# Optimization experiments

Measured on AMD Instinct MI355X. Metric: run time of the kernel, lower is better.

The kernel has to match this reference:

```python
import jax, jax.numpy as jnp
import numpy as np

HEADS = 12
KEY_DIM = 16
B, C, H, W = 16, 384, 64, 64


def _hard_swish(x):
    return x * jnp.clip(x + 3.0, 0.0, 6.0) / 6.0


def _affine(x, g, b):
    # Inference-mode BatchNorm folded into per-channel scale/shift (NCHW).
    return x * g[:, None, None] + b[:, None, None]


def _pw(x, w):
    # 1x1 conv as a channel contraction: x [B,Cin,H,W], w [Cout,Cin].
    return jnp.einsum('bchw,oc->bohw', x, w)


def setup_inputs() -> dict:
    key = jax.random.key(0)
    ks = jax.random.split(key, 20)
    d = {}
    d['x'] = jax.random.normal(ks[0], (B, C, H, W), dtype=jnp.float32)
    d['rnd_offset'] = jax.random.uniform(ks[1], (B, 2, 1, 1), dtype=jnp.float32) * 6.0 - 3.0
    S = HEADS * KEY_DIM  # 192
    d['proj_w'] = jax.random.normal(ks[2], (3 * S, C + 2), dtype=jnp.float32) * 0.05
    d['proj_g'] = jax.random.uniform(ks[3], (3 * S,), dtype=jnp.float32) + 0.5
    d['proj_b'] = jax.random.normal(ks[4], (3 * S,), dtype=jnp.float32) * 0.1
    d['vp2_w'] = jax.random.normal(ks[5], (C, S), dtype=jnp.float32) * 0.05
    d['vp2_g'] = jax.random.uniform(ks[6], (C,), dtype=jnp.float32) + 0.5
    d['vp2_b'] = jax.random.normal(ks[7], (C,), dtype=jnp.float32) * 0.1
    d['dw_w'] = jax.random.normal(ks[8], (C, 1, 5, 5), dtype=jnp.float32) * 0.1
    d['dw_g'] = jax.random.uniform(ks[9], (C,), dtype=jnp.float32) + 0.5
    d['dw_b'] = jax.random.normal(ks[10], (C,), dtype=jnp.float32) * 0.1
    d['pw1_w'] = jax.random.normal(ks[11], (4 * C, C), dtype=jnp.float32) * 0.05
    d['pw1_g'] = jax.random.uniform(ks[12], (4 * C,), dtype=jnp.float32) + 0.5
    d['pw1_b'] = jax.random.normal(ks[13], (4 * C,), dtype=jnp.float32) * 0.1
    d['pw2_w'] = jax.random.normal(ks[14], (C, 4 * C), dtype=jnp.float32) * 0.05
    d['out_g'] = jax.random.uniform(ks[15], (C,), dtype=jnp.float32) + 0.5
    d['out_b'] = jax.random.normal(ks[16], (C,), dtype=jnp.float32) * 0.1
    d['rz_attn'] = jnp.float32(0.1)
    d['rz_ffn'] = jnp.float32(0.1)
    d['embed_strength'] = jnp.float32(-10.0)
    return d


def reference(x, rnd_offset, proj_w, proj_g, proj_b, vp2_w, vp2_g, vp2_b,
              dw_w, dw_g, dw_b, pw1_w, pw1_g, pw1_b, pw2_w, out_g, out_b,
              rz_attn, rz_ffn, embed_strength):
    b, c, h, w = x.shape
    # --- learned-strength positional embedding with random per-image offset ---
    xp = jnp.arange(w, dtype=x.dtype) / 1000.0
    yp = jnp.arange(h, dtype=x.dtype) / 1000.0
    xx, yy = jnp.meshgrid(xp, yp, indexing='xy')      # each (H, W)
    pos = jnp.stack([xx, yy], axis=0)[None]           # (1, 2, H, W)
    pos = jnp.exp(embed_strength) * (pos + rnd_offset)  # (B, 2, H, W)
    x_emb = jnp.concatenate([x, pos], axis=1)         # (B, C+2, H, W)

    # --- qkv projection (1x1 conv + BN + ReLU), computed in fp32 ---
    proj = jax.nn.relu(_affine(_pw(x_emb, proj_w), proj_g, proj_b))
    proj = proj.astype(jnp.float32)

    S = HEADS * KEY_DIM
    N = h * w

    def get_slice(i):
        # (B, S, H, W) slice -> (B*heads, N, key_dim)
        s = proj[:, i * S:(i + 1) * S]
        return s.reshape(b * HEADS, KEY_DIM, N).transpose(0, 2, 1)

    q, k, v = get_slice(0), get_slice(1), get_slice(2)

    # --- non-causal linear attention: Q (K^T V) / (Q sum(K)) ---
    ktv = jnp.einsum('bnd,bne->bde', k, v)            # (B*heads, d, d)
    numer = jnp.einsum('bnd,bde->bne', q, ktv)        # (B*heads, N, d)
    denom = jnp.einsum('bnd,bd->bn', q, k.sum(axis=1))[..., None]  # (B*heads, N, 1)
    out = numer / jnp.maximum(denom, 1e-4)
    out = out.transpose(0, 2, 1).reshape(b, S, h, w)  # (B, heads*key_dim, H, W)

    # --- value projection back to channels ---
    out = jax.nn.relu(_affine(_pw(out, vp2_w), vp2_g, vp2_b))
    y = x + rz_attn * out

    # --- FFN: depthwise 5x5 -> expand 1x1 -> project 1x1 (+ BNs) ---
    z = jax.lax.conv_general_dilated(
        y, dw_w, window_strides=(1, 1), padding='SAME',
        dimension_numbers=('NCHW', 'OIHW', 'NCHW'), feature_group_count=c)
    z = _hard_swish(_affine(z, dw_g, dw_b))
    z = _hard_swish(_affine(_pw(z, pw1_w), pw1_g, pw1_b))
    z = _affine(_pw(z, pw2_w), out_g, out_b)
    return y + rz_ffn * z
```

## Files before the change

kernel.cpp:

```cpp
#include <hip/hip_runtime.h>
#include <cstdint>

typedef unsigned short u16;
typedef __attribute__((ext_vector_type(8))) __bf16 bf16x8;
typedef __attribute__((ext_vector_type(4))) float f32x4;

__device__ __forceinline__ u16 f2bf(float f) {
    union { float f; uint32_t u; } v; v.f = f;
    uint32_t u = v.u;
    uint32_t r = (u + 0x7fffu + ((u >> 16) & 1u)) >> 16;
    return (u16)r;
}
__device__ __forceinline__ float bf2f(u16 h) {
    union { uint32_t u; float f; } v; v.u = ((uint32_t)h) << 16;
    return v.f;
}

__device__ __forceinline__ void ld_lds16(const u16* g, u16* l) {
    __builtin_amdgcn_global_load_lds(
        (const __attribute__((address_space(1))) uint32_t*)g,
        (__attribute__((address_space(3))) uint32_t*)l, 16, 0, 0);
}

__global__ __launch_bounds__(256) void prep(
    const float* __restrict__ proj_w, const float* __restrict__ proj_g,
    const float* __restrict__ proj_b, const float* __restrict__ vp2_w,
    const float* __restrict__ pw1_w, const float* __restrict__ pw2_w,
    const float* __restrict__ dw_w,
    u16* __restrict__ w1p, u16* __restrict__ w2, u16* __restrict__ w3,
    u16* __restrict__ w4, float* __restrict__ gp, float2* __restrict__ dwp)
{
    int i = blockIdx.x * 256 + threadIdx.x;
    if (i < 245760) {
        int o = i / 384, k = i - o * 384;
        w1p[i] = (o < 576) ? f2bf(proj_w[o * 386 + k]) : (u16)0;
        return;
    }
    i -= 245760;
    if (i < 73728) { w2[i] = f2bf(vp2_w[i]); return; }
    i -= 73728;
    if (i < 589824) { w3[i] = f2bf(pw1_w[i]); return; }
    i -= 589824;
    if (i < 589824) { w4[i] = f2bf(pw2_w[i]); return; }
    i -= 589824;
    if (i < 2560) {
        int which = i / 640, o = i - which * 640;
        float v = 0.f;
        if (o < 576) {
            v = (which == 0) ? proj_g[o] : (which == 1) ? proj_b[o]
                : (which == 2) ? proj_w[o * 386 + 384] : proj_w[o * 386 + 385];
        }
        gp[i] = v; return;
    }
    i -= 2560;
    if (i < 4800) {
        int tap = i / 192, cp = i - tap * 192;
        dwp[i] = make_float2(dw_w[(2 * cp) * 25 + tap], dw_w[(2 * cp + 1) * 25 + tap]);
    }
}

__global__ __launch_bounds__(256) void transpose_x(const float* __restrict__ x,
                                                   u16* __restrict__ xt)
{
    __shared__ float tile[64][65];
    int b = blockIdx.x, n0 = blockIdx.y * 64, c0 = blockIdx.z * 64;
    int t = threadIdx.x;
    int jj = t & 63, i0 = t >> 6;
    #pragma unroll
    for (int r = 0; r < 16; r++) {
        int ci = r * 4 + i0;
        tile[ci][jj] = x[((size_t)b * 384 + c0 + ci) * 4096 + n0 + jj];
    }
    __syncthreads();
    #pragma unroll
    for (int r = 0; r < 16; r++) {
        int ni = r * 4 + i0;
        xt[(size_t)(b * 4096 + n0 + ni) * 384 + c0 + jj] = f2bf(tile[jj][ni]);
    }
}

__global__ __launch_bounds__(256) void transpose_out(const u16* __restrict__ zf,
                                                     float* __restrict__ out)
{
    __shared__ float tile[64][65];
    int b = blockIdx.x, n0 = blockIdx.y * 64, c0 = blockIdx.z * 64;
    int t = threadIdx.x;
    int jj = t & 63, i0 = t >> 6;
    #pragma unroll
    for (int r = 0; r < 16; r++) {
        int ni = r * 4 + i0;
        tile[ni][jj] = bf2f(zf[(size_t)(b * 4096 + n0 + ni) * 384 + c0 + jj]);
    }
    __syncthreads();
    #pragma unroll
    for (int r = 0; r < 16; r++) {
        int ci = r * 4 + i0;
        out[((size_t)b * 384 + c0 + ci) * 4096 + n0 + jj] = tile[jj][ci];
    }
}

template <int MODE>
__global__ __launch_bounds__(256) void gemm_nhwc(
    const u16* __restrict__ A, const u16* __restrict__ W,
    u16* __restrict__ out, int K, int Osz,
    const float* __restrict__ g, const float* __restrict__ bb,
    const float* __restrict__ w1x, const float* __restrict__ w1y,
    const u16* __restrict__ res, const float* __restrict__ sc,
    const float* __restrict__ rnd)
{
    constexpr int BK = 32;
    __shared__ u16 sA[2][128 * BK];
    __shared__ u16 sB[2][128 * BK];
    const int tid = threadIdx.x;
    const int lane = tid & 63;
    const int wv = tid >> 6;
    const int wm = (wv >> 1) * 64;
    const int wn = (wv & 1) * 64;
    const int m0 = blockIdx.x * 128;
    const int o0 = blockIdx.y * 128;
    const int q = lane >> 4;
    const int mr = lane & 15;

    const int tq = tid >> 2;
    const int tk = (tid & 3) * 8;
    const size_t ga0 = (size_t)(m0 + tq) * K + tk;
    const size_t ga1 = (size_t)(m0 + 64 + tq) * K + tk;
    const size_t gb0 = (size_t)(o0 + tq) * K + tk;
    const size_t gb1 = (size_t)(o0 + 64 + tq) * K + tk;
    const int lo0 = tq * BK + tk;
    const int lo1 = (64 + tq) * BK + tk;

    f32x4 acc[4][4] = {};

    ld_lds16(A + ga0, &sA[0][lo0]);
    ld_lds16(A + ga1, &sA[0][lo1]);
    ld_lds16(W + gb0, &sB[0][lo0]);
    ld_lds16(W + gb1, &sB[0][lo1]);

    int buf = 0;
    for (int k0 = 0; k0 < K; k0 += BK) {
        __syncthreads();
        if (k0 + BK < K) {
            ld_lds16(A + ga0 + k0 + BK, &sA[buf ^ 1][lo0]);
            ld_lds16(A + ga1 + k0 + BK, &sA[buf ^ 1][lo1]);
            ld_lds16(W + gb0 + k0 + BK, &sB[buf ^ 1][lo0]);
            ld_lds16(W + gb1 + k0 + BK, &sB[buf ^ 1][lo1]);
        }
        bf16x8 af[4], bfr[4];
        #pragma unroll
        for (int i = 0; i < 4; i++)
            af[i] = *(const bf16x8*)&sA[buf][(wm + i * 16 + mr) * BK + q * 8];
        #pragma unroll
        for (int j = 0; j < 4; j++)
            bfr[j] = *(const bf16x8*)&sB[buf][(wn + j * 16 + mr) * BK + q * 8];
        #pragma unroll
        for (int i = 0; i < 4; i++)
            #pragma unroll
            for (int j = 0; j < 4; j++)
                acc[i][j] = __builtin_amdgcn_mfma_f32_16x16x32_bf16(af[i], bfr[j], acc[i][j], 0, 0, 0);
        buf ^= 1;
    }

    float E = 0.f, offx = 0.f, offy = 0.f, rz = 0.f;
    if constexpr (MODE == 1) {
        E = expf(sc[0]);
        int bimg = m0 >> 12;
        offx = rnd[bimg * 2 + 0];
        offy = rnd[bimg * 2 + 1];
    }
    if constexpr (MODE == 2 || MODE == 4) rz = sc[0];

    #pragma unroll
    for (int j = 0; j < 4; j++) {
        int o = o0 + wn + j * 16 + mr;
        float gg = g[o], bbv = bb[o];
        float wx = 0.f, wy = 0.f;
        if constexpr (MODE == 1) { wx = w1x[o]; wy = w1y[o]; }
        #pragma unroll
        for (int i = 0; i < 4; i++) {
            #pragma unroll
            for (int r = 0; r < 4; r++) {
                int pix = m0 + wm + i * 16 + q * 4 + r;
                float v = acc[i][j][r];
                if constexpr (MODE == 1) {
                    int n = pix & 4095;
                    float px = E * ((float)(n & 63) * 0.001f + offx);
                    float py = E * ((float)(n >> 6) * 0.001f + offy);
                    v += px * wx + py * wy;
                    v = fmaxf(gg * v + bbv, 0.f);
                } else if constexpr (MODE == 2) {
                    v = fmaxf(gg * v + bbv, 0.f);
                    v = bf2f(res[(size_t)pix * 384 + o]) + rz * v;
                } else if constexpr (MODE == 3) {
                    float t = gg * v + bbv;
                    v = t * fminf(fmaxf(t + 3.f, 0.f), 6.f) * (1.f / 6.f);
                } else {
                    float t = gg * v + bbv;
                    v = bf2f(res[(size_t)pix * 384 + o]) + rz * t;
                }
                out[(size_t)pix * Osz + o] = f2bf(v);
            }
        }
    }
}

__global__ __launch_bounds__(256) void attn_ktv(const u16* __restrict__ proj,
                                                float* __restrict__ ktvp)
{
    int bh = blockIdx.x;
    int ch = blockIdx.y;
    int b = bh / 12, h = bh - b * 12;
    const u16* base = proj + (size_t)b * 4096 * 640;
    int kc = 192 + h * 16, vc = 384 + h * 16;
    __shared__ u16 ks[256 * 16];
    __shared__ u16 vs[256 * 16];
    int t = threadIdx.x;
    int d = t >> 4, e = t & 15;
    float acc = 0.f, ksum = 0.f;
    for (int n0 = ch * 1024; n0 < ch * 1024 + 1024; n0 += 256) {
        __syncthreads();
        const u16* r = base + (size_t)(n0 + t) * 640;
        ((float4*)&ks[t * 16])[0] = ((const float4*)(r + kc))[0];
        ((float4*)&ks[t * 16])[1] = ((const float4*)(r + kc))[1];
        ((float4*)&vs[t * 16])[0] = ((const float4*)(r + vc))[0];
        ((float4*)&vs[t * 16])[1] = ((const float4*)(r + vc))[1];
        __syncthreads();
        #pragma unroll 8
        for (int n = 0; n < 256; n++)
            acc += bf2f(ks[n * 16 + d]) * bf2f(vs[n * 16 + e]);
        if (t < 16) {
            #pragma unroll 8
            for (int n = 0; n < 256; n++) ksum += bf2f(ks[n * 16 + t]);
        }
    }
    float* o = ktvp + ((size_t)bh * 4 + ch) * 272;
    o[t] = acc;
    if (t < 16) o[256 + t] = ksum;
}

__global__ __launch_bounds__(256) void attn_apply(const u16* __restrict__ proj,
                                                  const float* __restrict__ ktvp,
                                                  u16* __restrict__ att)
{
    int bh = blockIdx.x;
    int b = bh / 12, h = bh - b * 12;
    __shared__ float kt[272];
    int t = threadIdx.x;
    {
        const float* p = ktvp + (size_t)bh * 4 * 272;
        kt[t] = p[t] + p[272 + t] + p[544 + t] + p[816 + t];
        if (t < 16) {
            int u = 256 + t;
            kt[u] = p[u] + p[272 + u] + p[544 + u] + p[816 + u];
        }
    }
    __syncthreads();
    int n = blockIdx.y * 256 + t;
    const u16* qr = proj + (size_t)(b * 4096 + n) * 640 + h * 16;
    float qv[16];
    #pragma unroll
    for (int d = 0; d < 16; d++) qv[d] = bf2f(qr[d]);
    float denom = 0.f;
    #pragma unroll
    for (int d = 0; d < 16; d++) denom += qv[d] * kt[256 + d];
    float rcp = 1.f / fmaxf(denom, 1e-4f);
    u16* op = att + (size_t)(b * 4096 + n) * 192 + h * 16;
    #pragma unroll
    for (int e = 0; e < 16; e++) {
        float s = 0.f;
        #pragma unroll
        for (int d = 0; d < 16; d++) s += qv[d] * kt[d * 16 + e];
        op[e] = f2bf(s * rcp);
    }
}

__global__ __launch_bounds__(192) void dwconv(const u16* __restrict__ y,
                                              const float2* __restrict__ wt,
                                              const float* __restrict__ g,
                                              const float* __restrict__ bc,
                                              u16* __restrict__ z)
{
    const int cp = threadIdx.x;
    const int xc = blockIdx.x;
    const int b  = blockIdx.y;
    const int c0 = cp * 2;

    float2 wv[25];
    #pragma unroll
    for (int t = 0; t < 25; t++) wv[t] = wt[t * 192 + cp];
    const float g0 = g[c0], g1 = g[c0 + 1];
    const float b0 = bc[c0], b1 = bc[c0 + 1];

    const size_t ibase = (size_t)b * 4096;
    const u16* ycol = y + ibase * 384 + c0;

    uint32_t r0[5], r1[5], r2[5], r3[5], r4[5];

#define LOADROW(yy, dst)                                                     \
    {                                                                        \
        if ((unsigned)(yy) < 64u) {                                          \
            const u16* rp = ycol + (size_t)(yy) * 64 * 384;                  \
            _Pragma("unroll")                                                \
            for (int dx = 0; dx < 5; dx++) {                                 \
                int xx = xc + dx - 2;                                        \
                dst[dx] = ((unsigned)xx < 64u)                               \
                              ? *(const uint32_t*)(rp + (size_t)xx * 384)    \
                              : 0u;                                          \
            }                                                                \
        } else {                                                             \
            _Pragma("unroll")                                                \
            for (int dx = 0; dx < 5; dx++) dst[dx] = 0u;                     \
        }                                                                    \
    }

#define COMPUTE(yr, A, B, C, D, E)                                           \
    if ((yr) < 64) {                                                         \
        float a0 = 0.f, a1 = 0.f;                                            \
        _Pragma("unroll")                                                    \
        for (int dx = 0; dx < 5; dx++) {                                     \
            uint32_t p;                                                      \
            p = A[dx];                                                       \
            a0 += wv[dx].x * bf2f((u16)(p & 0xffffu));                       \
            a1 += wv[dx].y * bf2f((u16)(p >> 16));                           \
            p = B[dx];                                                       \
            a0 += wv[5 + dx].x * bf2f((u16)(p & 0xffffu));                   \
            a1 += wv[5 + dx].y * bf2f((u16)(p >> 16));                       \
            p = C[dx];                                                       \
            a0 += wv[10 + dx].x * bf2f((u16)(p & 0xffffu));                  \
            a1 += wv[10 + dx].y * bf2f((u16)(p >> 16));                      \
            p = D[dx];                                                       \
            a0 += wv[15 + dx].x * bf2f((u16)(p & 0xffffu));                  \
            a1 += wv[15 + dx].y * bf2f((u16)(p >> 16));                      \
            p = E[dx];                                                       \
            a0 += wv[20 + dx].x * bf2f((u16)(p & 0xffffu));                  \
            a1 += wv[20 + dx].y * bf2f((u16)(p >> 16));                      \
        }                                                                    \
        float t0 = g0 * a0 + b0;                                             \
        float t1 = g1 * a1 + b1;                                             \
        t0 = t0 * fminf(fmaxf(t0 + 3.f, 0.f), 6.f) * (1.f / 6.f);            \
        t1 = t1 * fminf(fmaxf(t1 + 3.f, 0.f), 6.f) * (1.f / 6.f);            \
        uint32_t packed = (uint32_t)f2bf(t0) | ((uint32_t)f2bf(t1) << 16);   \
        *(uint32_t*)(z + (ibase + (size_t)(yr) * 64 + xc) * 384 + c0) = packed; \
    }

#define STEP(yr, A, B, C, D, E)                                              \
    COMPUTE(yr, A, B, C, D, E)                                               \
    LOADROW((yr) + 3, A)

    LOADROW(-2, r0)
    LOADROW(-1, r1)
    LOADROW(0, r2)
    LOADROW(1, r3)
    LOADROW(2, r4)

    for (int base = 0; base < 65; base += 5) {
        STEP(base + 0, r0, r1, r2, r3, r4)
        STEP(base + 1, r1, r2, r3, r4, r0)
        STEP(base + 2, r2, r3, r4, r0, r1)
        STEP(base + 3, r3, r4, r0, r1, r2)
        STEP(base + 4, r4, r0, r1, r2, r3)
    }
#undef STEP
#undef COMPUTE
#undef LOADROW
}

extern "C" void kernel_launch(void* const* d_in, const int* in_sizes, int n_in,
                              void* d_out, int out_size, void* d_ws, size_t ws_size,
                              hipStream_t stream)
{
    (void)in_sizes; (void)n_in; (void)out_size; (void)ws_size;
    const float* x       = (const float*)d_in[0];
    const float* rnd     = (const float*)d_in[1];
    const float* proj_w  = (const float*)d_in[2];
    const float* proj_g  = (const float*)d_in[3];
    const float* proj_b  = (const float*)d_in[4];
    const float* vp2_w   = (const float*)d_in[5];
    const float* vp2_g   = (const float*)d_in[6];
    const float* vp2_b   = (const float*)d_in[7];
    const float* dw_w    = (const float*)d_in[8];
    const float* dw_g    = (const float*)d_in[9];
    const float* dw_b    = (const float*)d_in[10];
    const float* pw1_w   = (const float*)d_in[11];
    const float* pw1_g   = (const float*)d_in[12];
    const float* pw1_b   = (const float*)d_in[13];
    const float* pw2_w   = (const float*)d_in[14];
    const float* out_g   = (const float*)d_in[15];
    const float* out_b   = (const float*)d_in[16];
    const float* rz_attn = (const float*)d_in[17];
    const float* rz_ffn  = (const float*)d_in[18];
    const float* es      = (const float*)d_in[19];
    float* out = (float*)d_out;

    char* ws = (char*)d_ws;
    u16*   xt   = (u16*)(ws + 0);
    u16*   att  = (u16*)(ws + 50331648);
    u16*   z2   = (u16*)(ws + 0);
    u16*   proj = (u16*)(ws + 201326592);
    u16*   z1   = proj;
    u16*   z4   = proj;
    u16*   yt   = (u16*)(ws + 285212672);
    u16*   w1p  = (u16*)(ws + 335753216);
    u16*   w2   = (u16*)(ws + 336244736);
    u16*   w3   = (u16*)(ws + 336392192);
    u16*   w4   = (u16*)(ws + 337571840);
    float* gp   = (float*)(ws + 338751488);
    float2* dwp = (float2*)(ws + 338761728);
    float* ktvp = (float*)(ws + 338800128);

    prep<<<5885, 256, 0, stream>>>(proj_w, proj_g, proj_b, vp2_w, pw1_w, pw2_w,
                                   dw_w, w1p, w2, w3, w4, gp, dwp);
    transpose_x<<<dim3(16, 64, 6), 256, 0, stream>>>(x, xt);
    gemm_nhwc<1><<<dim3(512, 5), 256, 0, stream>>>(xt, w1p, proj, 384, 640,
        gp, gp + 640, gp + 1280, gp + 1920, nullptr, es, rnd);
    attn_ktv<<<dim3(192, 4), 256, 0, stream>>>(proj, ktvp);
    attn_apply<<<dim3(192, 16), 256, 0, stream>>>(proj, ktvp, att);
    gemm_nhwc<2><<<dim3(512, 3), 256, 0, stream>>>(att, w2, yt, 192, 384,
        vp2_g, vp2_b, nullptr, nullptr, xt, rz_attn, nullptr);
    dwconv<<<dim3(64, 16), 192, 0, stream>>>(yt, dwp, dw_g, dw_b, z1);
    gemm_nhwc<3><<<dim3(512, 12), 256, 0, stream>>>(z1, w3, z2, 384, 1536,
        pw1_g, pw1_b, nullptr, nullptr, nullptr, nullptr, nullptr);
    gemm_nhwc<4><<<dim3(512, 3), 256, 0, stream>>>(z2, w4, z4, 1536, 384,
        out_g, out_b, nullptr, nullptr, yt, rz_ffn, nullptr);
    transpose_out<<<dim3(16, 64, 6), 256, 0, stream>>>(z4, out);
}
```

Measured before the change: 768.2 us.

## Triple-buffer GEMM LDS loads, swizzle LDS layout, remap blocks across XCDs

The NHWC GEMM moves from a double-buffered to a triple-buffered LDS pipeline. Loads are issued two k-steps ahead, with explicit vmcnt waits and a raw barrier. The LDS layout is XOR-swizzled on the k-slot to reduce bank conflicts on the fragment reads. The 2D grid is flattened to 1D with an XCD-aware block remap (stride of 8), so neighbouring tiles land on the same chiplet for better L2 reuse. In exchange, LDS use rises by half, and the hand-written waitcnt logic is fragile.

```diff
diff --git a/kernel.cpp b/kernel.cpp
--- a/kernel.cpp
+++ b/kernel.cpp
@@ -102,63 +102,84 @@
 template <int MODE>
 __global__ __launch_bounds__(256) void gemm_nhwc(
     const u16* __restrict__ A, const u16* __restrict__ W,
-    u16* __restrict__ out, int K, int Osz,
+    u16* __restrict__ out, int K, int Osz, int nOT,
     const float* __restrict__ g, const float* __restrict__ bb,
     const float* __restrict__ w1x, const float* __restrict__ w1y,
     const u16* __restrict__ res, const float* __restrict__ sc,
     const float* __restrict__ rnd)
 {
     constexpr int BK = 32;
-    __shared__ u16 sA[2][128 * BK];
-    __shared__ u16 sB[2][128 * BK];
+    __shared__ u16 sA[3][128 * BK];
+    __shared__ u16 sB[3][128 * BK];
     const int tid = threadIdx.x;
     const int lane = tid & 63;
     const int wv = tid >> 6;
     const int wm = (wv >> 1) * 64;
     const int wn = (wv & 1) * 64;
-    const int m0 = blockIdx.x * 128;
-    const int o0 = blockIdx.y * 128;
+
+    const int nwg = gridDim.x;
+    const int q8 = nwg >> 3;
+    const int b1 = (blockIdx.x & 7) * q8 + (blockIdx.x >> 3);
+    const int mt = b1 / nOT;
+    const int ot = b1 - mt * nOT;
+    const int m0 = mt * 128;
+    const int o0 = ot * 128;
+
     const int q = lane >> 4;
     const int mr = lane & 15;
+    const int ks = (q ^ ((mr >> 1) & 3)) * 8;
 
     const int tq = tid >> 2;
-    const int tk = (tid & 3) * 8;
+    const int sl = tid & 3;
+    const int tk = (sl ^ ((tq >> 1) & 3)) * 8;
     const size_t ga0 = (size_t)(m0 + tq) * K + tk;
     const size_t ga1 = (size_t)(m0 + 64 + tq) * K + tk;
     const size_t gb0 = (size_t)(o0 + tq) * K + tk;
     const size_t gb1 = (size_t)(o0 + 64 + tq) * K + tk;
-    const int lo0 = tq * BK + tk;
-    const int lo1 = (64 + tq) * BK + tk;
+    const int lo0 = tq * BK + sl * 8;
+    const int lo1 = (64 + tq) * BK + sl * 8;
 
     f32x4 acc[4][4] = {};
+    const int nIter = K >> 5;
 
     ld_lds16(A + ga0, &sA[0][lo0]);
     ld_lds16(A + ga1, &sA[0][lo1]);
     ld_lds16(W + gb0, &sB[0][lo0]);
     ld_lds16(W + gb1, &sB[0][lo1]);
+    if (nIter > 1) {
+        ld_lds16(A + ga0 + BK, &sA[1][lo0]);
+        ld_lds16(A + ga1 + BK, &sA[1][lo1]);
+        ld_lds16(W + gb0 + BK, &sB[1][lo0]);
+        ld_lds16(W + gb1 + BK, &sB[1][lo1]);
+    }
 
     int buf = 0;
-    for (int k0 = 0; k0 < K; k0 += BK) {
-        __syncthreads();
-        if (k0 + BK < K) {
-            ld_lds16(A + ga0 + k0 + BK, &sA[buf ^ 1][lo0]);
-            ld_lds16(A + ga1 + k0 + BK, &sA[buf ^ 1][lo1]);
-            ld_lds16(W + gb0 + k0 + BK, &sB[buf ^ 1][lo0]);
-            ld_lds16(W + gb1 + k0 + BK, &sB[buf ^ 1][lo1]);
+    for (int t = 0; t < nIter; ++t) {
+        if (t + 1 < nIter) asm volatile("s_waitcnt vmcnt(4)" ::: "memory");
+        else               asm volatile("s_waitcnt vmcnt(0)" ::: "memory");
+        __builtin_amdgcn_s_barrier();
+        __builtin_amdgcn_sched_barrier(0);
+        if (t + 2 < nIter) {
+            int nb = buf - 1; if (nb < 0) nb += 3;
+            int k2 = (t + 2) * BK;
+            ld_lds16(A + ga0 + k2, &sA[nb][lo0]);
+            ld_lds16(A + ga1 + k2, &sA[nb][lo1]);
+            ld_lds16(W + gb0 + k2, &sB[nb][lo0]);
+            ld_lds16(W + gb1 + k2, &sB[nb][lo1]);
         }
         bf16x8 af[4], bfr[4];
         #pragma unroll
         for (int i = 0; i < 4; i++)
-            af[i] = *(const bf16x8*)&sA[buf][(wm + i * 16 + mr) * BK + q * 8];
+            af[i] = *(const bf16x8*)&sA[buf][(wm + i * 16 + mr) * BK + ks];
         #pragma unroll
         for (int j = 0; j < 4; j++)
-            bfr[j] = *(const bf16x8*)&sB[buf][(wn + j * 16 + mr) * BK + q * 8];
+            bfr[j] = *(const bf16x8*)&sB[buf][(wn + j * 16 + mr) * BK + ks];
         #pragma unroll
         for (int i = 0; i < 4; i++)
             #pragma unroll
             for (int j = 0; j < 4; j++)
                 acc[i][j] = __builtin_amdgcn_mfma_f32_16x16x32_bf16(af[i], bfr[j], acc[i][j], 0, 0, 0);
-        buf ^= 1;
+        buf++; if (buf == 3) buf = 0;
     }
 
     float E = 0.f, offx = 0.f, offy = 0.f, rz = 0.f;
@@ -411,16 +432,16 @@
     prep<<<5885, 256, 0, stream>>>(proj_w, proj_g, proj_b, vp2_w, pw1_w, pw2_w,
                                    dw_w, w1p, w2, w3, w4, gp, dwp);
     transpose_x<<<dim3(16, 64, 6), 256, 0, stream>>>(x, xt);
-    gemm_nhwc<1><<<dim3(512, 5), 256, 0, stream>>>(xt, w1p, proj, 384, 640,
+    gemm_nhwc<1><<<2560, 256, 0, stream>>>(xt, w1p, proj, 384, 640, 5,
         gp, gp + 640, gp + 1280, gp + 1920, nullptr, es, rnd);
     attn_ktv<<<dim3(192, 4), 256, 0, stream>>>(proj, ktvp);
     attn_apply<<<dim3(192, 16), 256, 0, stream>>>(proj, ktvp, att);
-    gemm_nhwc<2><<<dim3(512, 3), 256, 0, stream>>>(att, w2, yt, 192, 384,
+    gemm_nhwc<2><<<1536, 256, 0, stream>>>(att, w2, yt, 192, 384, 3,
         vp2_g, vp2_b, nullptr, nullptr, xt, rz_attn, nullptr);
     dwconv<<<dim3(64, 16), 192, 0, stream>>>(yt, dwp, dw_g, dw_b, z1);
-    gemm_nhwc<3><<<dim3(512, 12), 256, 0, stream>>>(z1, w3, z2, 384, 1536,
+    gemm_nhwc<3><<<6144, 256, 0, stream>>>(z1, w3, z2, 384, 1536, 12,
         pw1_g, pw1_b, nullptr, nullptr, nullptr, nullptr, nullptr);
-    gemm_nhwc<4><<<dim3(512, 3), 256, 0, stream>>>(z2, w4, z4, 1536, 384,
+    gemm_nhwc<4><<<1536, 256, 0, stream>>>(z2, w4, z4, 1536, 384, 3,
         out_g, out_b, nullptr, nullptr, yt, rz_ffn, nullptr);
     transpose_out<<<dim3(16, 64, 6), 256, 0, stream>>>(z4, out);
 }
```

New measurement: 726.4 us. 1.06x faster.
